# Kernel tuning notes

Hardware: AMD Instinct MI355X
Metric: run time of the kernel (lower is better)

The kernel has to match this reference:

```python
import jax, jax.numpy as jnp
import numpy as np

B, T, F = 16, 1024, 512       # batch, time, input_dim
G, V, D = 2, 320, 128         # num_groups, num_vars, var_dim (quantized_dim // G)
TAU = 2.0                     # max_temp * decay**0 at num_updates=0
EPS = 1e-7


def setup_inputs() -> dict:
    key = jax.random.key(0)
    kx, kw, kc, kg = jax.random.split(key, 4)
    x = jax.random.normal(kx, (B, T, F), dtype=jnp.float32)
    w_proj = jax.random.normal(kw, (G * V, F), dtype=jnp.float32)  # NormalLinear: std=1
    b_proj = jnp.zeros((G * V,), dtype=jnp.float32)
    codebook = jax.random.uniform(kc, (1, G * V, D), dtype=jnp.float32)  # uniform init
    u = jax.random.uniform(kg, (B * T, G, V), dtype=jnp.float32, minval=1e-10, maxval=1.0)
    gumbel = -jnp.log(-jnp.log(u))
    return {"x": x, "w_proj": w_proj, "b_proj": b_proj, "codebook": codebook, "gumbel": gumbel}


def reference(x, w_proj, b_proj, codebook, gumbel):
    bsz, tsz, _ = x.shape
    # projection -> (B, T, G, V)
    logits = (jnp.einsum("btf,nf->btn", x, w_proj) + b_proj).reshape(bsz, tsz, G, V)

    # hard one-hot of argmax (float32), like scatter_
    k = jnp.argmax(logits, axis=-1)
    hard_x = jax.nn.one_hot(k, V, dtype=jnp.float32)  # (B, T, G, V)

    # code perplexity: mean over batch dim only, sum over (T, G)
    hard_probs = hard_x.mean(axis=0)  # (T, G, V)
    code_perplexity = jnp.exp(-jnp.sum(hard_probs * jnp.log(hard_probs + EPS), axis=-1)).sum()

    # prob perplexity: softmax over codes, mean over all tokens, sum over groups
    flat_logits = logits.reshape(bsz * tsz, G, V)
    avg_probs = jax.nn.softmax(flat_logits, axis=-1).mean(axis=0)  # (G, V)
    prob_perplexity = jnp.exp(-jnp.sum(avg_probs * jnp.log(avg_probs + EPS), axis=-1)).sum()

    # gumbel-softmax, hard=True with straight-through estimator (training path)
    y_soft = jax.nn.softmax((flat_logits + gumbel) / TAU, axis=-1)  # (N, G, V)
    idx = jnp.argmax(y_soft, axis=-1)
    y_hard = jax.nn.one_hot(idx, V, dtype=y_soft.dtype)
    y = y_hard + y_soft - jax.lax.stop_gradient(y_soft)  # (N, G, V)

    # broadcast-multiply + sum over codes == grouped gather/matmul against codebook
    cb_gvd = codebook.reshape(G, V, D)
    quantized = jnp.einsum("ngv,gvd->ngd", y, cb_gvd).reshape(bsz, tsz, G * D)
    return quantized, code_perplexity, prob_perplexity
```

## Files before the change

kernel.cpp:

```cpp
#include <hip/hip_runtime.h>
#include <math.h>

#define B_   16
#define T_   1024
#define F_   512
#define G_   2
#define V_   320
#define D_   128
#define N_   (B_ * T_)
#define GV   (G_ * V_)
#define EPS_ 1e-7f

#define ROWS    64
#define THREADS 512
#define NBLK    (N_ / ROWS)
#define NC      32

typedef _Float16 half8 __attribute__((ext_vector_type(8)));
typedef float f32x16 __attribute__((ext_vector_type(16)));

#define CNTW      (T_ * G_ * (V_ / 2))
#define WS_COUNTS 0
#define WS_AVG    CNTW
#define WS_ENT    (WS_AVG + NBLK * GV)
#define WS_WPK    (WS_ENT + T_ * G_)
#define WS_AVGRED (WS_WPK + (GV * F_ * 2 / 2))

__global__ __launch_bounds__(640) void k_conv_w(
    const float* __restrict__ w, _Float16* __restrict__ wpk,
    unsigned* __restrict__ counts)
{
  const int cl = blockIdx.x;
  const int c = cl >> 1, limb = cl & 1;
#pragma unroll
  for (int z = 0; z < 8; ++z)
    counts[(size_t)z * 40960 + blockIdx.x * 640 + threadIdx.x] = 0u;
#pragma unroll
  for (int it = 0; it < 2; ++it) {
    const int t2 = threadIdx.x + it * 640;
    const int m = t2 >> 6, ln = t2 & 63;
    const int row = m * 32 + (ln & 31);
    const int k0 = c * 16 + (ln >> 5) * 8;
    const float4 v0 = *(const float4*)(w + (size_t)row * F_ + k0);
    const float4 v1 = *(const float4*)(w + (size_t)row * F_ + k0 + 4);
    half8 h;
#pragma unroll
    for (int k = 0; k < 8; ++k) {
      const float vk = (k < 4) ? ((const float*)&v0)[k] : ((const float*)&v1)[k - 4];
      const _Float16 hk = (_Float16)vk;
      h[k] = limb ? (_Float16)((vk - (float)hk) * 2048.0f) : hk;
    }
    ((half8*)wpk)[((size_t)cl * 20 + m) * 64 + ln] = h;
  }
}

__global__ __launch_bounds__(THREADS, 1) void k_fused(
    const float* __restrict__ x, const _Float16* __restrict__ wpk,
    const float* __restrict__ bias, const float* __restrict__ cb,
    const float* __restrict__ gum, float* __restrict__ out,
    unsigned* __restrict__ counts, float* __restrict__ avg_part)
{
  __shared__ float SB2[16 * GV];
  const int tid = threadIdx.x;
  const int wv  = tid >> 6;
  const int ln  = tid & 63;
  const int lo  = ln & 31, hi = ln >> 5;
  const int wvm = wv >> 2, wvn = wv & 3;
  const int blk = blockIdx.x;
  const int n0  = blk * ROWS;

  f32x16 ah_acc[5], al_acc[5];
#pragma unroll
  for (int t = 0; t < 5; ++t)
#pragma unroll
    for (int i = 0; i < 16; ++i) { ah_acc[t][i] = 0.0f; al_acc[t][i] = 0.0f; }

  const half8* wbase = (const half8*)wpk + (size_t)(wvn * 5) * 64 + ln;
  const float* xrow  = x + (size_t)(n0 + wvm * 32 + lo) * F_ + hi * 8;

  half8 wch[5], wcl[5];
#pragma unroll
  for (int t = 0; t < 5; ++t) {
    wch[t] = wbase[(size_t)(0 * 20 + t) * 64];
    wcl[t] = wbase[(size_t)(1 * 20 + t) * 64];
  }
  float4 xc0 = *(const float4*)(xrow + 0);
  float4 xc1 = *(const float4*)(xrow + 4);

  for (int cc = 0; cc < NC; ++cc) {
    const int c1 = (cc + 1 < NC) ? cc + 1 : cc;
    half8 wnh[5], wnl[5];
#pragma unroll
    for (int t = 0; t < 5; ++t) {
      wnh[t] = wbase[((size_t)(c1 * 2 + 0) * 20 + t) * 64];
      wnl[t] = wbase[((size_t)(c1 * 2 + 1) * 20 + t) * 64];
    }
    const float4 xn0 = *(const float4*)(xrow + c1 * 16);
    const float4 xn1 = *(const float4*)(xrow + c1 * 16 + 4);

    half8 xh8, xl8;
#pragma unroll
    for (int k = 0; k < 8; ++k) {
      const float f = (k < 4) ? ((const float*)&xc0)[k] : ((const float*)&xc1)[k - 4];
      const _Float16 h = (_Float16)f;
      xh8[k] = h;
      xl8[k] = (_Float16)((f - (float)h) * 2048.0f);
    }
#pragma unroll
    for (int t = 0; t < 5; ++t) {
      ah_acc[t] = __builtin_amdgcn_mfma_f32_32x32x16_f16(xh8, wch[t], ah_acc[t], 0, 0, 0);
      al_acc[t] = __builtin_amdgcn_mfma_f32_32x32x16_f16(xl8, wch[t], al_acc[t], 0, 0, 0);
      al_acc[t] = __builtin_amdgcn_mfma_f32_32x32x16_f16(xh8, wcl[t], al_acc[t], 0, 0, 0);
    }
#pragma unroll
    for (int t = 0; t < 5; ++t) { wch[t] = wnh[t]; wcl[t] = wnl[t]; }
    xc0 = xn0; xc1 = xn1;
  }

  float bfrag[5];
#pragma unroll
  for (int t = 0; t < 5; ++t) bfrag[t] = bias[wvn * 160 + t * 32 + lo];

  float racc[G_][5];
#pragma unroll
  for (int g = 0; g < G_; ++g)
#pragma unroll
    for (int j = 0; j < 5; ++j) racc[g][j] = 0.f;

  float* LBUF = SB2;

#pragma unroll
  for (int R = 0; R < 4; ++R) {
    if (wvm == (R >> 1)) {
#pragma unroll
      for (int t = 0; t < 5; ++t) {
        const int col = wvn * 160 + t * 32 + lo;
#pragma unroll
        for (int rr = 0; rr < 8; ++rr) {
          const int reg  = ((R & 1) << 3) + rr;
          const int lrow = (rr & 3) + ((rr >> 2) << 3) + (hi << 2);
          LBUF[lrow * GV + col] =
              ah_acc[t][reg] + al_acc[t][reg] * (1.0f / 2048.0f) + bfrag[t];
        }
      }
    }
    __syncthreads();
#pragma unroll
    for (int rr2 = 0; rr2 < 2; ++rr2) {
      const int lrow = wv * 2 + rr2;
      const int n = n0 + R * 16 + lrow;
#pragma unroll
      for (int g = 0; g < G_; ++g) {
        float L[5], GU[5];
#pragma unroll
        for (int j = 0; j < 5; ++j) {
          L[j]  = LBUF[lrow * GV + g * V_ + 64 * j + ln];
          GU[j] = gum[(size_t)n * GV + g * V_ + 64 * j + ln];
        }
        float m1 = L[0];         int a1 = ln;
        float m2 = L[0] + GU[0]; int a2 = ln;
#pragma unroll
        for (int j = 1; j < 5; ++j) {
          const int cix = 64 * j + ln;
          if (L[j] > m1) { m1 = L[j]; a1 = cix; }
          const float t2 = L[j] + GU[j];
          if (t2 > m2) { m2 = t2; a2 = cix; }
        }
        for (int off = 32; off; off >>= 1) {
          float om = __shfl_down(m1, off); int oa = __shfl_down(a1, off);
          if (om > m1 || (om == m1 && oa < a1)) { m1 = om; a1 = oa; }
          float om2 = __shfl_down(m2, off); int oa2 = __shfl_down(a2, off);
          if (om2 > m2 || (om2 == m2 && oa2 < a2)) { m2 = om2; a2 = oa2; }
        }
        m1 = __shfl(m1, 0); a1 = __shfl(a1, 0); a2 = __shfl(a2, 0);

        float e[5], s = 0.f;
#pragma unroll
        for (int j = 0; j < 5; ++j) { e[j] = expf(L[j] - m1); s += e[j]; }
        for (int off = 32; off; off >>= 1) s += __shfl_down(s, off);
        s = __shfl(s, 0);
        const float inv = 1.0f / s;
#pragma unroll
        for (int j = 0; j < 5; ++j) racc[g][j] += e[j] * inv;

        if (ln == 0) {
          const int t = n & (T_ - 1);
          atomicAdd(&counts[(t * G_ + g) * (V_ / 2) + (a1 >> 1)],
                    1u << ((a1 & 1) * 16));
        }
        const float2* cbr = (const float2*)(cb + (size_t)(g * V_ + a2) * D_);
        float2* op = (float2*)(out + (size_t)n * (G_ * D_) + g * D_);
        op[ln] = cbr[ln];
      }
    }
    __syncthreads();
  }

  float* la = SB2;
#pragma unroll
  for (int g = 0; g < G_; ++g)
#pragma unroll
    for (int j = 0; j < 5; ++j)
      la[wv * GV + g * V_ + 64 * j + ln] = racc[g][j];
  __syncthreads();
  for (int cix = tid; cix < GV; cix += THREADS) {
    float s = 0.f;
#pragma unroll
    for (int v = 0; v < 8; ++v) s += la[v * GV + cix];
    avg_part[(size_t)blk * GV + cix] = s;
  }
}

__global__ __launch_bounds__(256) void k_post(
    const unsigned* __restrict__ counts, float* __restrict__ ent,
    const float* __restrict__ avg_part, float* __restrict__ avgred)
{
  const int b = blockIdx.x;
  const int lane = threadIdx.x & 63;
  if (b < (T_ * G_) / 4) {
    const int item = b * 4 + (threadIdx.x >> 6);
    const unsigned* c = counts + (size_t)item * (V_ / 2);
    float s = 0.f;
#pragma unroll
    for (int j = 0; j < 3; ++j) {
      const int wi = lane + 64 * j;
      if (wi < V_ / 2) {
        const unsigned wd = c[wi];
        const float h0 = (float)(wd & 0xffffu) * (1.0f / B_);
        const float h1 = (float)(wd >> 16) * (1.0f / B_);
        s += h0 * logf(h0 + EPS_) + h1 * logf(h1 + EPS_);
      }
    }
    for (int off = 32; off; off >>= 1) s += __shfl_down(s, off);
    if (lane == 0) ent[item] = expf(-s);
  } else {
    const int cix = (b - (T_ * G_) / 4) * 4 + (threadIdx.x >> 6);
    float s = 0.f;
    for (int bb = lane; bb < NBLK; bb += 64) s += avg_part[(size_t)bb * GV + cix];
    for (int off = 32; off; off >>= 1) s += __shfl_down(s, off);
    if (lane == 0) avgred[cix] = s;
  }
}

__global__ __launch_bounds__(GV) void k_final(
    const float* __restrict__ avgred, const float* __restrict__ ent,
    float* __restrict__ out2)
{
  __shared__ float sh[GV];
  __shared__ float shc[GV];
  const int tid = threadIdx.x;

  const float p = avgred[tid] * (1.0f / N_);
  sh[tid] = p * logf(p + EPS_);

  float cs = 0.f;
  for (int i = tid; i < T_ * G_; i += GV) cs += ent[i];
  shc[tid] = cs;
  __syncthreads();

  if (tid < 64) {
    float s0 = 0.f, s1 = 0.f, sc = 0.f;
    for (int j = tid; j < V_; j += 64) { s0 += sh[j]; s1 += sh[V_ + j]; }
    for (int j = tid; j < GV; j += 64) sc += shc[j];
    for (int off = 32; off; off >>= 1) {
      s0 += __shfl_down(s0, off);
      s1 += __shfl_down(s1, off);
      sc += __shfl_down(sc, off);
    }
    if (tid == 0) {
      out2[0] = sc;
      out2[1] = expf(-s0) + expf(-s1);
    }
  }
}

extern "C" void kernel_launch(void* const* d_in, const int* in_sizes, int n_in,
                              void* d_out, int out_size, void* d_ws, size_t ws_size,
                              hipStream_t stream) {
  const float* x   = (const float*)d_in[0];
  const float* w   = (const float*)d_in[1];
  const float* b   = (const float*)d_in[2];
  const float* cb  = (const float*)d_in[3];
  const float* gum = (const float*)d_in[4];
  float* out = (float*)d_out;
  float* ws  = (float*)d_ws;

  unsigned* counts = (unsigned*)(ws + WS_COUNTS);
  float* avgp   = ws + WS_AVG;
  float* ent    = ws + WS_ENT;
  _Float16* wpk = (_Float16*)(ws + WS_WPK);
  float* avgred = ws + WS_AVGRED;

  k_conv_w<<<64, 640, 0, stream>>>(w, wpk, counts);
  k_fused<<<NBLK, THREADS, 0, stream>>>(x, wpk, b, cb, gum, out, counts, avgp);
  k_post<<<(T_ * G_) / 4 + GV / 4, 256, 0, stream>>>(counts, ent, avgp, avgred);
  k_final<<<1, GV, 0, stream>>>(avgred, ent, out + (size_t)N_ * G_ * D_);
}
```

Measured before the change: 185.8 us.

## Stage split-fp16 x tile in LDS and reorder GEMM loop per output tile

The x row tile is converted once into hi/lo fp16 limbs and stored in a 128 KB shared buffer, instead of each wave re-reading and re-converting x from global memory every k-chunk. The GEMM loop is restructured to iterate over output tiles outermost, so only one low-limb accumulator is live at a time and it is folded into the main accumulator at the end, cutting register pressure. MFMA groups are wrapped in s_setprio to favour matrix issue. The cost is a large LDS footprint, an extra sync, and weight fragments re-fetched per tile with less prefetch depth.

```diff
diff --git a/kernel.cpp b/kernel.cpp
--- a/kernel.cpp
+++ b/kernel.cpp
@@ -17,6 +17,7 @@
 #define NC      32
 
 typedef _Float16 half8 __attribute__((ext_vector_type(8)));
+typedef _Float16 half4 __attribute__((ext_vector_type(4)));
 typedef float f32x16 __attribute__((ext_vector_type(16)));
 
 #define CNTW      (T_ * G_ * (V_ / 2))
@@ -60,7 +61,7 @@
     const float* __restrict__ gum, float* __restrict__ out,
     unsigned* __restrict__ counts, float* __restrict__ avg_part)
 {
-  __shared__ float SB2[16 * GV];
+  __shared__ __align__(16) unsigned char SB[131072];
   const int tid = threadIdx.x;
   const int wv  = tid >> 6;
   const int ln  = tid & 63;
@@ -69,53 +70,80 @@
   const int blk = blockIdx.x;
   const int n0  = blk * ROWS;
 
-  f32x16 ah_acc[5], al_acc[5];
+  {
+    const int row = tid >> 3, kq = tid & 7;
+    const float* xr = x + (size_t)(n0 + row) * F_;
+    const int rbase = ((row >> 5) * 1024) + ((row & 31) * 16);
+#pragma unroll
+    for (int it = 0; it < 16; ++it) {
+      const int k0 = it * 32 + kq * 4;
+      const float4 v = *(const float4*)(xr + k0);
+      half4 hh, hl;
+#pragma unroll
+      for (int k = 0; k < 4; ++k) {
+        const float f = ((const float*)&v)[k];
+        const _Float16 h = (_Float16)f;
+        hh[k] = h;
+        hl[k] = (_Float16)((f - (float)h) * 2048.0f);
+      }
+      const int ad = (k0 >> 4) * 2048 + rbase + ((k0 >> 3) & 1) * 512 + (k0 & 7) * 2;
+      *(half4*)(SB + ad) = hh;
+      *(half4*)(SB + 65536 + ad) = hl;
+    }
+  }
+  __syncthreads();
+
+  f32x16 ah[5];
 #pragma unroll
   for (int t = 0; t < 5; ++t)
 #pragma unroll
-    for (int i = 0; i < 16; ++i) { ah_acc[t][i] = 0.0f; al_acc[t][i] = 0.0f; }
-
-  const half8* wbase = (const half8*)wpk + (size_t)(wvn * 5) * 64 + ln;
-  const float* xrow  = x + (size_t)(n0 + wvm * 32 + lo) * F_ + hi * 8;
-
-  half8 wch[5], wcl[5];
+    for (int i = 0; i < 16; ++i) ah[t][i] = 0.0f;
+
+  const half8* wp8 = (const half8*)wpk;
+  const int xoff = wvm * 1024 + ln * 16;
+
 #pragma unroll
   for (int t = 0; t < 5; ++t) {
-    wch[t] = wbase[(size_t)(0 * 20 + t) * 64];
-    wcl[t] = wbase[(size_t)(1 * 20 + t) * 64];
-  }
-  float4 xc0 = *(const float4*)(xrow + 0);
-  float4 xc1 = *(const float4*)(xrow + 4);
-
-  for (int cc = 0; cc < NC; ++cc) {
-    const int c1 = (cc + 1 < NC) ? cc + 1 : cc;
-    half8 wnh[5], wnl[5];
-#pragma unroll
-    for (int t = 0; t < 5; ++t) {
-      wnh[t] = wbase[((size_t)(c1 * 2 + 0) * 20 + t) * 64];
-      wnl[t] = wbase[((size_t)(c1 * 2 + 1) * 20 + t) * 64];
-    }
-    const float4 xn0 = *(const float4*)(xrow + c1 * 16);
-    const float4 xn1 = *(const float4*)(xrow + c1 * 16 + 4);
-
-    half8 xh8, xl8;
-#pragma unroll
-    for (int k = 0; k < 8; ++k) {
-      const float f = (k < 4) ? ((const float*)&xc0)[k] : ((const float*)&xc1)[k - 4];
-      const _Float16 h = (_Float16)f;
-      xh8[k] = h;
-      xl8[k] = (_Float16)((f - (float)h) * 2048.0f);
-    }
-#pragma unroll
-    for (int t = 0; t < 5; ++t) {
-      ah_acc[t] = __builtin_amdgcn_mfma_f32_32x32x16_f16(xh8, wch[t], ah_acc[t], 0, 0, 0);
-      al_acc[t] = __builtin_amdgcn_mfma_f32_32x32x16_f16(xl8, wch[t], al_acc[t], 0, 0, 0);
-      al_acc[t] = __builtin_amdgcn_mfma_f32_32x32x16_f16(xh8, wcl[t], al_acc[t], 0, 0, 0);
-    }
-#pragma unroll
-    for (int t = 0; t < 5; ++t) { wch[t] = wnh[t]; wcl[t] = wnl[t]; }
-    xc0 = xn0; xc1 = xn1;
-  }
+    const int g0 = wvn * 5 + t;
+    f32x16 al;
+#pragma unroll
+    for (int i = 0; i < 16; ++i) al[i] = 0.0f;
+
+    half8 wAh = wp8[(size_t)(0 * 40 + g0) * 64 + ln];
+    half8 wAl = wp8[(size_t)(0 * 40 + 20 + g0) * 64 + ln];
+    half8 wBh = wp8[(size_t)(1 * 40 + g0) * 64 + ln];
+    half8 wBl = wp8[(size_t)(1 * 40 + 20 + g0) * 64 + ln];
+    half8 xAh = *(const half8*)(SB + 0 * 2048 + xoff);
+    half8 xAl = *(const half8*)(SB + 65536 + 0 * 2048 + xoff);
+
+    for (int c = 0; c < NC; c += 2) {
+      half8 xBh = *(const half8*)(SB + (c + 1) * 2048 + xoff);
+      half8 xBl = *(const half8*)(SB + 65536 + (c + 1) * 2048 + xoff);
+      __builtin_amdgcn_s_setprio(1);
+      ah[t] = __builtin_amdgcn_mfma_f32_32x32x16_f16(xAh, wAh, ah[t], 0, 0, 0);
+      al    = __builtin_amdgcn_mfma_f32_32x32x16_f16(xAl, wAh, al,    0, 0, 0);
+      al    = __builtin_amdgcn_mfma_f32_32x32x16_f16(xAh, wAl, al,    0, 0, 0);
+      __builtin_amdgcn_s_setprio(0);
+      if (c + 2 < NC) {
+        wAh = wp8[(size_t)((c + 2) * 40 + g0) * 64 + ln];
+        wAl = wp8[(size_t)((c + 2) * 40 + 20 + g0) * 64 + ln];
+        xAh = *(const half8*)(SB + (c + 2) * 2048 + xoff);
+        xAl = *(const half8*)(SB + 65536 + (c + 2) * 2048 + xoff);
+      }
+      __builtin_amdgcn_s_setprio(1);
+      ah[t] = __builtin_amdgcn_mfma_f32_32x32x16_f16(xBh, wBh, ah[t], 0, 0, 0);
+      al    = __builtin_amdgcn_mfma_f32_32x32x16_f16(xBl, wBh, al,    0, 0, 0);
+      al    = __builtin_amdgcn_mfma_f32_32x32x16_f16(xBh, wBl, al,    0, 0, 0);
+      __builtin_amdgcn_s_setprio(0);
+      if (c + 3 < NC) {
+        wBh = wp8[(size_t)((c + 3) * 40 + g0) * 64 + ln];
+        wBl = wp8[(size_t)((c + 3) * 40 + 20 + g0) * 64 + ln];
+      }
+    }
+#pragma unroll
+    for (int i = 0; i < 16; ++i) ah[t][i] += al[i] * (1.0f / 2048.0f);
+  }
+  __syncthreads();
 
   float bfrag[5];
 #pragma unroll
@@ -127,7 +155,7 @@
 #pragma unroll
     for (int j = 0; j < 5; ++j) racc[g][j] = 0.f;
 
-  float* LBUF = SB2;
+  float* LBUF = (float*)SB;
 
 #pragma unroll
   for (int R = 0; R < 4; ++R) {
@@ -139,8 +167,7 @@
         for (int rr = 0; rr < 8; ++rr) {
           const int reg  = ((R & 1) << 3) + rr;
           const int lrow = (rr & 3) + ((rr >> 2) << 3) + (hi << 2);
-          LBUF[lrow * GV + col] =
-              ah_acc[t][reg] + al_acc[t][reg] * (1.0f / 2048.0f) + bfrag[t];
+          LBUF[lrow * GV + col] = ah[t][reg] + bfrag[t];
         }
       }
     }
@@ -196,7 +223,7 @@
     __syncthreads();
   }
 
-  float* la = SB2;
+  float* la = (float*)SB;
 #pragma unroll
   for (int g = 0; g < G_; ++g)
 #pragma unroll
```

Result: faster. 176.7 us (-4.9%).
